# Optimization experiments

Measured on AMD Instinct MI355X. Metric: run time of the kernel, lower is better.

Reference implementation:

```python
import jax, jax.numpy as jnp
import numpy as np

VAR_NUM = 96
EMBED_TIME = 128
INPUT_DIM = VAR_NUM * 2 + EMBED_TIME  # 320
ATTN_DIM = 64
N_HEADS = 8
ALL_DIM = ATTN_DIM * N_HEADS  # 512
B, N = 8, 2048
NEG_INF = -1e9  # finite stand-in for masked_fill(-inf); safe under softmax


def setup_inputs() -> dict:
    key = jax.random.key(0)
    ks = jax.random.split(key, 16)
    s = lambda d: 1.0 / np.sqrt(d)
    return {
        "times_in": jax.random.uniform(ks[0], (B, N), jnp.float32),
        "data_in": jax.random.normal(ks[1], (B, N, VAR_NUM), jnp.float32),
        "mask_in": jnp.ones((B, N, VAR_NUM), jnp.float32),
        "exist_times": jax.random.randint(ks[2], (B, N), 0, 2, jnp.int32),
        # TimeEmbedding params
        "w_per": jax.random.normal(ks[3], (1, EMBED_TIME - 1), jnp.float32),
        "b_per": jnp.zeros((EMBED_TIME - 1,), jnp.float32),
        "w_lin": jax.random.normal(ks[4], (1, 1), jnp.float32),
        "b_lin": jnp.zeros((1,), jnp.float32),
        # Attention params
        "Wq": jax.random.normal(ks[5], (INPUT_DIM, ALL_DIM), jnp.float32) * s(INPUT_DIM),
        "bq": jnp.zeros((ALL_DIM,), jnp.float32),
        "Wk": jax.random.normal(ks[6], (INPUT_DIM, ALL_DIM), jnp.float32) * s(INPUT_DIM),
        "bk": jnp.zeros((ALL_DIM,), jnp.float32),
        "Wv": jax.random.normal(ks[7], (INPUT_DIM, ALL_DIM), jnp.float32) * s(INPUT_DIM),
        "bv": jnp.zeros((ALL_DIM,), jnp.float32),
        "Wfc": jax.random.normal(ks[8], (ALL_DIM, ATTN_DIM), jnp.float32) * s(ALL_DIM),
        "bfc": jnp.zeros((ATTN_DIM,), jnp.float32),
    }


def reference(times_in, data_in, mask_in, exist_times,
              w_per, b_per, w_lin, b_lin,
              Wq, bq, Wk, bk, Wv, bv, Wfc, bfc):
    b, n = times_in.shape
    tt = times_in[..., None]  # [b, n, 1]
    # TimeEmbedding: [linear(tt), sin(periodic(tt))]
    te = jnp.concatenate([tt @ w_lin + b_lin, jnp.sin(tt @ w_per + b_per)], axis=-1)
    x = jnp.concatenate([data_in, mask_in, te], axis=-1)  # [b, n, INPUT_DIM]

    def heads(w, bias):
        return (x @ w + bias).reshape(b, n, N_HEADS, ATTN_DIM).transpose(0, 2, 1, 3)

    q, k, v = heads(Wq, bq), heads(Wk, bk), heads(Wv, bv)  # [b, h, n, d]
    # NOTE: custom scale uses sqrt(input_dim), not sqrt(head_dim)
    scores = jnp.einsum("bhqd,bhkd->bhqk", q, k) / jnp.sqrt(jnp.float32(INPUT_DIM))
    m = (exist_times != 0)
    scores = jnp.where(m[:, None, None, :], scores, NEG_INF)  # mask keys
    attn = jax.nn.softmax(scores, axis=-1)  # dropout p=0 in eval reference
    out = jnp.einsum("bhqk,bhkd->bhqd", attn, v)
    out = jnp.where(m[:, None, :, None], out, 0.0)  # zero masked query rows
    out = out.transpose(0, 2, 1, 3).reshape(b, n, ALL_DIM)
    return out @ Wfc + bfc  # [b, n, ATTN_DIM]
```

## Files before the change

### kernel.cpp

```cpp
#include <hip/hip_runtime.h>

#define N_ 2048
#define BN 16384
#define IN_DIM 320
#define QKV_N 1536
#define ALPHA 0.08064911f

typedef float f32x4 __attribute__((ext_vector_type(4)));
typedef short v8s __attribute__((ext_vector_type(8)));
typedef unsigned int u32x2 __attribute__((ext_vector_type(2)));

__device__ __forceinline__ short f2b(float f) {
  unsigned u = __builtin_bit_cast(unsigned, f);
  u = u + 0x7fff + ((u >> 16) & 1);
  return (short)(u >> 16);
}

__device__ __forceinline__ int piperm(int t) {
  return ((t >> 5) & 1) * 32 + ((t >> 2) & 3) * 8 + ((t >> 4) & 1) * 4 + (t & 3);
}

__global__ void build_x(const float* __restrict__ times, const float* __restrict__ data,
                        const float* __restrict__ maskv, const float* __restrict__ w_per,
                        const float* __restrict__ b_per, const float* __restrict__ w_lin,
                        const float* __restrict__ b_lin, short* __restrict__ x) {
  int row = blockIdx.x;
  int t = threadIdx.x;
  float tt = times[row];
  short* xr = x + (size_t)row * IN_DIM;
  const float* dr = data + (size_t)row * 96;
  const float* mr = maskv + (size_t)row * 96;
  if (t < 96) { xr[t] = f2b(dr[t]); xr[96 + t] = f2b(mr[t]); }
  float val;
  if (t == 0) val = tt * w_lin[0] + b_lin[0];
  else        val = __sinf(tt * w_per[t - 1] + b_per[t - 1]);
  xr[192 + t] = f2b(val);
}

__global__ void scan_mask(const int* __restrict__ exist, int* __restrict__ prefix,
                          int* __restrict__ ntg, int* __restrict__ totals,
                          short* __restrict__ flagsc) {
  __shared__ int sums[256];
  int b = blockIdx.x;
  int t = threadIdx.x;
  const int* e = exist + b * 2048;
  int loc[8];
  int s = 0;
#pragma unroll
  for (int j = 0; j < 8; ++j) { loc[j] = s; s += (e[t * 8 + j] != 0) ? 1 : 0; }
  sums[t] = s;
  __syncthreads();
  for (int d = 1; d < 256; d <<= 1) {
    int v = (t >= d) ? sums[t - d] : 0;
    __syncthreads();
    sums[t] += v;
    __syncthreads();
  }
  int total = sums[255];
  int base = (t == 0) ? 0 : sums[t - 1];
#pragma unroll
  for (int j = 0; j < 8; ++j) prefix[b * 2048 + t * 8 + j] = base + loc[j];
  if (t == 0) { ntg[b] = (total + 63) >> 6; totals[b] = total; }
#pragma unroll
  for (int j = 0; j < 8; ++j) {
    int slot = t * 8 + j;
    flagsc[b * 2048 + (slot & ~63) + piperm(slot & 63)] =
        (slot < total) ? (short)0x3F80 : (short)0;
  }
}

__global__ void transpose_w(const float* __restrict__ Wq, const float* __restrict__ Wk,
                            const float* __restrict__ Wv, const float* __restrict__ Wfc,
                            short* __restrict__ Wt, short* __restrict__ WfcT) {
  int idx = blockIdx.x * 256 + threadIdx.x;
  if (idx < QKV_N * IN_DIM) {
    int n = idx / IN_DIM, kk = idx - n * IN_DIM;
    const float* W = (n < 512) ? Wq : (n < 1024 ? Wk : Wv);
    Wt[idx] = f2b(W[(size_t)kk * 512 + (n & 511)]);
  } else {
    int j = idx - QKV_N * IN_DIM;
    int d = j >> 9, kk = j & 511;
    WfcT[j] = f2b(Wfc[kk * 64 + d]);
  }
}

__launch_bounds__(256)
__global__ void qkv_gemm(const short* __restrict__ x, const short* __restrict__ Wt,
                         const float* __restrict__ bq, const float* __restrict__ bk,
                         const float* __restrict__ bv, const int* __restrict__ exist,
                         const int* __restrict__ prefix,
                         short* __restrict__ q, short* __restrict__ kc, short* __restrict__ vc) {
  __shared__ short As[128][40];
  __shared__ short Bs[128][40];
  int bm = blockIdx.x;
  int bn = blockIdx.y;
  int tid = threadIdx.x, wave = tid >> 6, lane = tid & 63;
  int wm = wave >> 1, wn = wave & 1;
  int l16 = lane & 15, lh = lane >> 4;
  f32x4 acc[4][4] = {};
  for (int kt = 0; kt < 10; ++kt) {
    int k0 = kt * 32;
#pragma unroll
    for (int s = 0; s < 2; ++s) {
      int c = tid + s * 256;
      int r = c >> 2, c8 = c & 3;
      *(v8s*)&As[r][c8 * 8] = *(const v8s*)&x[(size_t)(bm * 128 + r) * IN_DIM + k0 + c8 * 8];
      *(v8s*)&Bs[r][c8 * 8] = *(const v8s*)&Wt[(size_t)(bn * 128 + r) * IN_DIM + k0 + c8 * 8];
    }
    __syncthreads();
    v8s af[4], bfr[4];
#pragma unroll
    for (int m = 0; m < 4; ++m) af[m] = *(const v8s*)&As[wm * 64 + m * 16 + l16][lh * 8];
#pragma unroll
    for (int n = 0; n < 4; ++n) bfr[n] = *(const v8s*)&Bs[wn * 64 + n * 16 + l16][lh * 8];
#pragma unroll
    for (int m = 0; m < 4; ++m)
#pragma unroll
      for (int n = 0; n < 4; ++n)
        acc[m][n] = __builtin_amdgcn_mfma_f32_16x16x32_bf16(af[m], bfr[n], acc[m][n], 0, 0, 0);
    __syncthreads();
  }
  int w = bn >> 2;
  if (w == 0) {
#pragma unroll
    for (int m = 0; m < 4; ++m) {
      int row0 = bm * 128 + wm * 64 + m * 16 + lh * 4;
#pragma unroll
      for (int n = 0; n < 4; ++n) {
        int c = (bn * 128 + wn * 64 + n * 16 + l16) & 511;
        float bb = bq[c];
        int h = c >> 6, d = c & 63;
#pragma unroll
        for (int r = 0; r < 4; ++r) {
          int rr = row0 + r;
          int b = rr >> 11, ntok = rr & 2047;
          q[(((size_t)(b * 8 + h) * N_ + ntok) << 6) + d] = f2b((acc[m][n][r] + bb) * ALPHA);
        }
      }
    }
  } else {
    short* dbuf = (w == 1) ? kc : vc;
    const float* bias = (w == 1) ? bk : bv;
#pragma unroll
    for (int m = 0; m < 4; ++m) {
      int row0 = bm * 128 + wm * 64 + m * 16 + lh * 4;
      int exr[4], dstr[4];
#pragma unroll
      for (int r = 0; r < 4; ++r) { exr[r] = exist[row0 + r]; dstr[r] = prefix[row0 + r]; }
      int b = row0 >> 11;
#pragma unroll
      for (int n = 0; n < 4; ++n) {
        int c = (bn * 128 + wn * 64 + n * 16 + l16) & 511;
        float bb = bias[c];
        int h = c >> 6, d = c & 63;
#pragma unroll
        for (int r = 0; r < 4; ++r)
          if (exr[r])
            dbuf[(((size_t)(b * 8 + h) * N_ + dstr[r]) << 6) + d] = f2b(acc[m][n][r] + bb);
      }
    }
  }
}

__launch_bounds__(256)
__global__ void fragmentize(short* __restrict__ kc, short* __restrict__ vc,
                            const int* __restrict__ ntg, const int* __restrict__ totals) {
  __shared__ short Ks[64][66];
  __shared__ short Vs[64][66];
  int bh = blockIdx.x;
  int b = bh >> 3;
  int nt = ntg[b], total = totals[b];
  int tid = threadIdx.x;
  size_t hb = (size_t)bh * N_ * 64;
  for (int tile = blockIdx.y; tile < nt; tile += 8) {
    int base = tile * 64;
#pragma unroll
    for (int s = 0; s < 2; ++s) {
      int c = tid + s * 256, r = c >> 3, c8 = c & 7;
      v8s kv = {0, 0, 0, 0, 0, 0, 0, 0};
      v8s vv = {0, 0, 0, 0, 0, 0, 0, 0};
      if (base + r < total) {
        kv = *(const v8s*)&kc[hb + (size_t)(base + r) * 64 + c8 * 8];
        vv = *(const v8s*)&vc[hb + (size_t)(base + r) * 64 + c8 * 8];
      }
      *(v8s*)&Ks[r][c8 * 8] = kv;
      *(v8s*)&Vs[r][c8 * 8] = vv;
    }
    __syncthreads();
#pragma unroll
    for (int s = 0; s < 2; ++s) {
      int c = tid + s * 256;
      int i = c >> 6, lh2 = (c >> 4) & 3, r16 = c & 15;
      *(v8s*)&kc[hb + (size_t)tile * 4096 + c * 8] =
          *(const v8s*)&Ks[(i >> 1) * 16 + r16][(i & 1) * 32 + lh2 * 8];
      int l16 = c & 15, lh = (c >> 4) & 3, kc2 = (c >> 6) & 1, n2 = c >> 7;
      int d = n2 * 16 + l16;
      v8s o;
#pragma unroll
      for (int jj = 0; jj < 8; ++jj) {
        int t2 = kc2 * 32 + (jj >> 2) * 16 + lh * 4 + (jj & 3);
        o[jj] = Vs[t2][d];
      }
      *(v8s*)&vc[hb + (size_t)tile * 4096 + c * 8] = o;
    }
    __syncthreads();
  }
}

__launch_bounds__(256, 2)
__global__ void attn_kernel(const short* __restrict__ q, const short* __restrict__ kT,
                            const short* __restrict__ vT, const short* __restrict__ flagsc,
                            const int* __restrict__ ntg, const int* __restrict__ exist,
                            short* __restrict__ att) {
  int bx = blockIdx.x;
  int bh = ((bx >> 6) << 3) | (bx & 7);
  int qblk = (bx >> 3) & 7;
  int b = bh >> 3, h = bh & 7;
  int tid = threadIdx.x, wave = tid >> 6, lane = tid & 63;
  int l16 = lane & 15, lh = lane >> 4;
  int q0 = qblk * 256 + wave * 64;
  int nt = ntg[b];
  const short* qp = q + (size_t)bh * N_ * 64;
  const short* kpt = kT + (size_t)bh * 131072;
  const short* vpt = vT + (size_t)bh * 131072;
  const short* fpt = flagsc + b * N_;
  const int* ex = exist + b * N_;
  v8s qf[4][2];
#pragma unroll
  for (int m = 0; m < 4; ++m)
#pragma unroll
    for (int kcx = 0; kcx < 2; ++kcx)
      qf[m][kcx] = *(const v8s*)&qp[(size_t)(q0 + m * 16 + l16) * 64 + kcx * 32 + lh * 8];
  f32x4 oacc[4][4] = {};
  f32x4 lacc[4] = {};
  const f32x4 zf = {0.f, 0.f, 0.f, 0.f};
  int voff = lane * 8;
  v8s kf[8], vf[8], ff[2];
#pragma unroll
  for (int i = 0; i < 8; ++i) {
    kf[i] = *(const v8s*)&kpt[i * 512 + voff];
    vf[i] = *(const v8s*)&vpt[i * 512 + voff];
  }
  ff[0] = *(const v8s*)&fpt[lh * 8];
  ff[1] = *(const v8s*)&fpt[32 + lh * 8];
#pragma unroll 1
  for (int kt = 0; kt < nt; ++kt) {
    const short* kn = kpt + (size_t)(kt + 1) * 4096;
    const short* vn = vpt + (size_t)(kt + 1) * 4096;
    const short* fn = fpt + (kt + 1) * 64;
    bool pre = (kt + 1 < nt);
#pragma unroll
    for (int mh = 0; mh < 2; ++mh) {
      f32x4 sacc[2][4];
#pragma unroll
      for (int n = 0; n < 4; ++n)
#pragma unroll
        for (int mm = 0; mm < 2; ++mm) {
          sacc[mm][n] = __builtin_amdgcn_mfma_f32_16x16x32_bf16(kf[n * 2], qf[mh * 2 + mm][0], zf, 0, 0, 0);
          sacc[mm][n] = __builtin_amdgcn_mfma_f32_16x16x32_bf16(kf[n * 2 + 1], qf[mh * 2 + mm][1], sacc[mm][n], 0, 0, 0);
        }
      if (mh == 1 && pre)
#pragma unroll
        for (int i = 0; i < 8; ++i) kf[i] = *(const v8s*)&kn[i * 512 + voff];
      v8s pf[2][2];
#pragma unroll
      for (int mm = 0; mm < 2; ++mm)
#pragma unroll
        for (int kcx = 0; kcx < 2; ++kcx)
#pragma unroll
          for (int half = 0; half < 2; ++half) {
            int n = kcx * 2 + half;
            float p0 = __builtin_amdgcn_exp2f(sacc[mm][n][0]);
            float p1 = __builtin_amdgcn_exp2f(sacc[mm][n][1]);
            float p2 = __builtin_amdgcn_exp2f(sacc[mm][n][2]);
            float p3 = __builtin_amdgcn_exp2f(sacc[mm][n][3]);
            uint w0, w1;
            asm("v_cvt_pk_bf16_f32 %0, %1, %2" : "=v"(w0) : "v"(p0), "v"(p1));
            asm("v_cvt_pk_bf16_f32 %0, %1, %2" : "=v"(w1) : "v"(p2), "v"(p3));
            ((uint*)&pf[mm][kcx])[half * 2]     = w0;
            ((uint*)&pf[mm][kcx])[half * 2 + 1] = w1;
          }
#pragma unroll
      for (int kcx = 0; kcx < 2; ++kcx) {
#pragma unroll
        for (int mm = 0; mm < 2; ++mm)
          lacc[mh * 2 + mm] = __builtin_amdgcn_mfma_f32_16x16x32_bf16(pf[mm][kcx], ff[kcx], lacc[mh * 2 + mm], 0, 0, 0);
#pragma unroll
        for (int n = 0; n < 4; ++n)
#pragma unroll
          for (int mm = 0; mm < 2; ++mm)
            oacc[mh * 2 + mm][n] = __builtin_amdgcn_mfma_f32_16x16x32_bf16(pf[mm][kcx], vf[n * 2 + kcx], oacc[mh * 2 + mm][n], 0, 0, 0);
      }
    }
    if (pre) {
#pragma unroll
      for (int i = 0; i < 8; ++i) vf[i] = *(const v8s*)&vn[i * 512 + voff];
      ff[0] = *(const v8s*)&fn[lh * 8];
      ff[1] = *(const v8s*)&fn[32 + lh * 8];
    }
  }
#pragma unroll
  for (int m = 0; m < 4; ++m)
#pragma unroll
    for (int r = 0; r < 4; ++r) {
      int row = q0 + m * 16 + lh * 4 + r;
      float qm = (ex[row] != 0) ? 1.f : 0.f;
      float inv = qm / fmaxf(lacc[m][r], 1e-20f);
#pragma unroll
      for (int n = 0; n < 4; ++n)
        att[((size_t)(b * N_ + row)) * 512 + h * 64 + n * 16 + l16] = f2b(oacc[m][n][r] * inv);
    }
}

__launch_bounds__(256)
__global__ void out_gemm(const short* __restrict__ att, const short* __restrict__ WfcT,
                         const float* __restrict__ bfc, float* __restrict__ out) {
  __shared__ short As[128][40];
  __shared__ short Bs[64][40];
  int bm = blockIdx.x;
  int tid = threadIdx.x, wave = tid >> 6, lane = tid & 63;
  int l16 = lane & 15, lh = lane >> 4;
  f32x4 acc[2][4] = {};
  for (int kt = 0; kt < 16; ++kt) {
    int k0 = kt * 32;
#pragma unroll
    for (int s = 0; s < 2; ++s) {
      int c = tid + s * 256;
      int r = c >> 2, c8 = c & 3;
      *(v8s*)&As[r][c8 * 8] = *(const v8s*)&att[(size_t)(bm * 128 + r) * 512 + k0 + c8 * 8];
    }
    { int r = tid >> 2, c8 = tid & 3;
      if (r < 64) *(v8s*)&Bs[r][c8 * 8] = *(const v8s*)&WfcT[(size_t)r * 512 + k0 + c8 * 8]; }
    __syncthreads();
    v8s bfr[4];
#pragma unroll
    for (int n = 0; n < 4; ++n) bfr[n] = *(const v8s*)&Bs[n * 16 + l16][lh * 8];
#pragma unroll
    for (int m = 0; m < 2; ++m) {
      v8s af = *(const v8s*)&As[wave * 32 + m * 16 + l16][lh * 8];
#pragma unroll
      for (int n = 0; n < 4; ++n)
        acc[m][n] = __builtin_amdgcn_mfma_f32_16x16x32_bf16(af, bfr[n], acc[m][n], 0, 0, 0);
    }
    __syncthreads();
  }
#pragma unroll
  for (int m = 0; m < 2; ++m)
#pragma unroll
    for (int n = 0; n < 4; ++n) {
      float bb = bfc[n * 16 + l16];
#pragma unroll
      for (int r = 0; r < 4; ++r) {
        int row = bm * 128 + wave * 32 + m * 16 + lh * 4 + r;
        out[(size_t)row * 64 + n * 16 + l16] = acc[m][n][r] + bb;
      }
    }
}

extern "C" void kernel_launch(void* const* d_in, const int* in_sizes, int n_in,
                              void* d_out, int out_size, void* d_ws, size_t ws_size,
                              hipStream_t stream) {
  const float* times = (const float*)d_in[0];
  const float* data  = (const float*)d_in[1];
  const float* maskv = (const float*)d_in[2];
  const int*   exist = (const int*)d_in[3];
  const float* w_per = (const float*)d_in[4];
  const float* b_per = (const float*)d_in[5];
  const float* w_lin = (const float*)d_in[6];
  const float* b_lin = (const float*)d_in[7];
  const float* Wq  = (const float*)d_in[8];
  const float* bq  = (const float*)d_in[9];
  const float* Wk  = (const float*)d_in[10];
  const float* bk  = (const float*)d_in[11];
  const float* Wv  = (const float*)d_in[12];
  const float* bv  = (const float*)d_in[13];
  const float* Wfc = (const float*)d_in[14];
  const float* bfc = (const float*)d_in[15];
  float* out = (float*)d_out;

  char* ws = (char*)d_ws;
  short* x     = (short*)(ws);
  short* Wt    = (short*)(ws + 10485760);
  short* WfcT  = (short*)(ws + 11468800);
  short* qb    = (short*)(ws + 11534336);
  short* kcb   = (short*)(ws + 28311552);
  short* vcb   = (short*)(ws + 45088768);
  short* att   = (short*)(ws + 61865984);
  short* flagsc= (short*)(ws + 78643200);
  int*   prefix= (int*)(ws + 78675968);
  int*   ntg   = (int*)(ws + 78741504);
  int*   totals= (int*)(ws + 78741536);

  build_x<<<BN, 128, 0, stream>>>(times, data, maskv, w_per, b_per, w_lin, b_lin, x);
  scan_mask<<<8, 256, 0, stream>>>(exist, prefix, ntg, totals, flagsc);
  transpose_w<<<2048, 256, 0, stream>>>(Wq, Wk, Wv, Wfc, Wt, WfcT);
  qkv_gemm<<<dim3(128, 12), 256, 0, stream>>>(x, Wt, bq, bk, bv, exist, prefix, qb, kcb, vcb);
  fragmentize<<<dim3(64, 8), 256, 0, stream>>>(kcb, vcb, ntg, totals);
  attn_kernel<<<512, 256, 0, stream>>>(qb, kcb, vcb, flagsc, ntg, exist, att);
  out_gemm<<<128, 256, 0, stream>>>(att, WfcT, bfc, out);
}
```

Before: 111.6 us.

## Pre-swizzle QKV GEMM operands into MFMA fragment layout and drop LDS staging

build_x and transpose_w now write x and the QKV weights directly in the per-lane MFMA fragment order (16-row by 32-k tiles). qkv_gemm then loads each operand fragment straight from global memory with one coalesced 16-byte load per lane. This removes the shared-memory staging and both barriers per k-step, and it prefetches the next k-tile's fragments into registers while the current MFMAs run. In exchange, both the A and B operands are read by several waves separately through global memory or cache instead of being shared in LDS, and the scattered writes in build_x and transpose_w may cost more.

Measured after the change: 109.6 us. Within noise of the previous version (-1.8%).

```diff
diff --git a/kernel.cpp b/kernel.cpp
--- a/kernel.cpp
+++ b/kernel.cpp
@@ -20,21 +20,30 @@
   return ((t >> 5) & 1) * 32 + ((t >> 2) & 3) * 8 + ((t >> 4) & 1) * 4 + (t & 3);
 }
 
+__device__ __forceinline__ size_t fragaddr(int ti, int r, int k) {
+  return (size_t)ti * 512 + ((k >> 3) & 3) * 128 + r * 8 + (k & 7);
+}
+
 __global__ void build_x(const float* __restrict__ times, const float* __restrict__ data,
                         const float* __restrict__ maskv, const float* __restrict__ w_per,
                         const float* __restrict__ b_per, const float* __restrict__ w_lin,
-                        const float* __restrict__ b_lin, short* __restrict__ x) {
+                        const float* __restrict__ b_lin, short* __restrict__ xF) {
   int row = blockIdx.x;
   int t = threadIdx.x;
   float tt = times[row];
-  short* xr = x + (size_t)row * IN_DIM;
+  int rt = row >> 4, l16r = row & 15;
   const float* dr = data + (size_t)row * 96;
   const float* mr = maskv + (size_t)row * 96;
-  if (t < 96) { xr[t] = f2b(dr[t]); xr[96 + t] = f2b(mr[t]); }
+  if (t < 96) {
+    xF[fragaddr(rt * 10 + (t >> 5), l16r, t & 31)] = f2b(dr[t]);
+    int k2 = 96 + t;
+    xF[fragaddr(rt * 10 + (k2 >> 5), l16r, k2 & 31)] = f2b(mr[t]);
+  }
   float val;
   if (t == 0) val = tt * w_lin[0] + b_lin[0];
   else        val = __sinf(tt * w_per[t - 1] + b_per[t - 1]);
-  xr[192 + t] = f2b(val);
+  int k3 = 192 + t;
+  xF[fragaddr(rt * 10 + (k3 >> 5), l16r, k3 & 31)] = f2b(val);
 }
 
 __global__ void scan_mask(const int* __restrict__ exist, int* __restrict__ prefix,
@@ -71,12 +80,13 @@
 
 __global__ void transpose_w(const float* __restrict__ Wq, const float* __restrict__ Wk,
                             const float* __restrict__ Wv, const float* __restrict__ Wfc,
-                            short* __restrict__ Wt, short* __restrict__ WfcT) {
+                            short* __restrict__ WtF, short* __restrict__ WfcT) {
   int idx = blockIdx.x * 256 + threadIdx.x;
   if (idx < QKV_N * IN_DIM) {
     int n = idx / IN_DIM, kk = idx - n * IN_DIM;
     const float* W = (n < 512) ? Wq : (n < 1024 ? Wk : Wv);
-    Wt[idx] = f2b(W[(size_t)kk * 512 + (n & 511)]);
+    WtF[fragaddr((n >> 4) * 10 + (kk >> 5), n & 15, kk & 31)] =
+        f2b(W[(size_t)kk * 512 + (n & 511)]);
   } else {
     int j = idx - QKV_N * IN_DIM;
     int d = j >> 9, kk = j & 511;
@@ -85,40 +95,38 @@
 }
 
 __launch_bounds__(256)
-__global__ void qkv_gemm(const short* __restrict__ x, const short* __restrict__ Wt,
+__global__ void qkv_gemm(const short* __restrict__ xF, const short* __restrict__ WtF,
                          const float* __restrict__ bq, const float* __restrict__ bk,
                          const float* __restrict__ bv, const int* __restrict__ exist,
                          const int* __restrict__ prefix,
                          short* __restrict__ q, short* __restrict__ kc, short* __restrict__ vc) {
-  __shared__ short As[128][40];
-  __shared__ short Bs[128][40];
   int bm = blockIdx.x;
   int bn = blockIdx.y;
   int tid = threadIdx.x, wave = tid >> 6, lane = tid & 63;
   int wm = wave >> 1, wn = wave & 1;
   int l16 = lane & 15, lh = lane >> 4;
+  int voff = lane * 8;
+  const short* ap = xF + (size_t)(bm * 8 + wm * 4) * 10 * 512;
+  const short* bp = WtF + (size_t)(bn * 8 + wn * 4) * 10 * 512;
   f32x4 acc[4][4] = {};
+  v8s af[4], bfr[4];
+#pragma unroll
+  for (int m = 0; m < 4; ++m) af[m] = *(const v8s*)&ap[(size_t)(m * 10) * 512 + voff];
+#pragma unroll
+  for (int n = 0; n < 4; ++n) bfr[n] = *(const v8s*)&bp[(size_t)(n * 10) * 512 + voff];
+#pragma unroll 1
   for (int kt = 0; kt < 10; ++kt) {
-    int k0 = kt * 32;
-#pragma unroll
-    for (int s = 0; s < 2; ++s) {
-      int c = tid + s * 256;
-      int r = c >> 2, c8 = c & 3;
-      *(v8s*)&As[r][c8 * 8] = *(const v8s*)&x[(size_t)(bm * 128 + r) * IN_DIM + k0 + c8 * 8];
-      *(v8s*)&Bs[r][c8 * 8] = *(const v8s*)&Wt[(size_t)(bn * 128 + r) * IN_DIM + k0 + c8 * 8];
-    }
-    __syncthreads();
-    v8s af[4], bfr[4];
-#pragma unroll
-    for (int m = 0; m < 4; ++m) af[m] = *(const v8s*)&As[wm * 64 + m * 16 + l16][lh * 8];
-#pragma unroll
-    for (int n = 0; n < 4; ++n) bfr[n] = *(const v8s*)&Bs[wn * 64 + n * 16 + l16][lh * 8];
 #pragma unroll
     for (int m = 0; m < 4; ++m)
 #pragma unroll
       for (int n = 0; n < 4; ++n)
         acc[m][n] = __builtin_amdgcn_mfma_f32_16x16x32_bf16(af[m], bfr[n], acc[m][n], 0, 0, 0);
-    __syncthreads();
+    if (kt < 9) {
+#pragma unroll
+      for (int m = 0; m < 4; ++m) af[m] = *(const v8s*)&ap[(size_t)(m * 10 + kt + 1) * 512 + voff];
+#pragma unroll
+      for (int n = 0; n < 4; ++n) bfr[n] = *(const v8s*)&bp[(size_t)(n * 10 + kt + 1) * 512 + voff];
+    }
   }
   int w = bn >> 2;
   if (w == 0) {
@@ -379,8 +387,8 @@
   float* out = (float*)d_out;
 
   char* ws = (char*)d_ws;
-  short* x     = (short*)(ws);
-  short* Wt    = (short*)(ws + 10485760);
+  short* xF    = (short*)(ws);
+  short* WtF   = (short*)(ws + 10485760);
   short* WfcT  = (short*)(ws + 11468800);
   short* qb    = (short*)(ws + 11534336);
   short* kcb   = (short*)(ws + 28311552);
@@ -391,10 +399,10 @@
   int*   ntg   = (int*)(ws + 78741504);
   int*   totals= (int*)(ws + 78741536);
 
-  build_x<<<BN, 128, 0, stream>>>(times, data, maskv, w_per, b_per, w_lin, b_lin, x);
+  build_x<<<BN, 128, 0, stream>>>(times, data, maskv, w_per, b_per, w_lin, b_lin, xF);
   scan_mask<<<8, 256, 0, stream>>>(exist, prefix, ntg, totals, flagsc);
-  transpose_w<<<2048, 256, 0, stream>>>(Wq, Wk, Wv, Wfc, Wt, WfcT);
-  qkv_gemm<<<dim3(128, 12), 256, 0, stream>>>(x, Wt, bq, bk, bv, exist, prefix, qb, kcb, vcb);
+  transpose_w<<<2048, 256, 0, stream>>>(Wq, Wk, Wv, Wfc, WtF, WfcT);
+  qkv_gemm<<<dim3(128, 12), 256, 0, stream>>>(xF, WtF, bq, bk, bv, exist, prefix, qb, kcb, vcb);
   fragmentize<<<dim3(64, 8), 256, 0, stream>>>(kcb, vcb, ntg, totals);
   attn_kernel<<<512, 256, 0, stream>>>(qb, kcb, vcb, flagsc, ntg, exist, att);
   out_gemm<<<128, 256, 0, stream>>>(att, WfcT, bfc, out);
```
